# Optimization experiments

Hardware: AMD Instinct MI355X
Metric: run time of the kernel (lower is better)

Reference implementation:

```python
import jax, jax.numpy as jnp
import numpy as np

E = 1024      # hidden_size
H = 16        # num_heads
D = E // H    # head_dim = 64
WIN = 256     # window_size
STRIDE = 128
G = 1         # global_tokens
B = 2
L = 4097      # seq_len; local_seq_len = 4096 tiles exactly into 31 windows


def setup_inputs() -> dict:
    key = jax.random.key(0)
    ks = jax.random.split(key, 9)
    s = 0.02
    return {
        "hidden_states": jax.random.normal(ks[0], (B, L, E), jnp.float32),
        "Wq": jax.random.normal(ks[1], (E, E), jnp.float32) * s,
        "bq": jnp.zeros((E,), jnp.float32),
        "Wk": jax.random.normal(ks[2], (E, E), jnp.float32) * s,
        "bk": jnp.zeros((E,), jnp.float32),
        "Wv": jax.random.normal(ks[3], (E, E), jnp.float32) * s,
        "bv": jnp.zeros((E,), jnp.float32),
        "Wo": jax.random.normal(ks[4], (E, E), jnp.float32) * s,
        "bo": jnp.zeros((E,), jnp.float32),
    }


def reference(hidden_states, Wq, bq, Wk, bk, Wv, bv, Wo, bo):
    b, seq_len, e = hidden_states.shape
    scale = 1.0 / jnp.sqrt(jnp.asarray(D, hidden_states.dtype))

    q = (hidden_states @ Wq + bq).reshape(b, seq_len, H, D)
    k = (hidden_states @ Wk + bk).reshape(b, seq_len, H, D)
    v = (hidden_states @ Wv + bv).reshape(b, seq_len, H, D)

    # ---- global tokens attend to the full sequence ----
    qg = q[:, :G]                                        # [b, G, H, D]
    gw = jnp.einsum('bghd,bshd->bhgs', qg, k) * scale    # [b, H, G, L]
    gp = jax.nn.softmax(gw, axis=-1)
    gctx = jnp.einsum('bhgs,bshd->bghd', gp, v).reshape(b, G, e)

    # ---- local windowed attention (overlapping strided windows) ----
    ql, kl, vl = q[:, G:], k[:, G:], v[:, G:]
    Lc = seq_len - G                                     # 4096
    num_windows = max(1, (Lc - WIN) // STRIDE + 1)       # 31
    starts = jnp.arange(num_windows) * STRIDE
    widx = starts[:, None] + jnp.arange(WIN)             # [W, w] window indices

    qw = ql[:, widx]                                     # [b, W, w, H, D]
    kw = kl[:, widx]
    vw = vl[:, widx]
    aw = jnp.einsum('bwqhd,bwkhd->bwhqk', qw, kw) * scale  # [b, W, H, w, w]
    ap = jax.nn.softmax(aw, axis=-1)
    ctx = jnp.einsum('bwhqk,bwkhd->bwqhd', ap, vw)       # [b, W, w, H, D]
    ctx = ctx.reshape(b, num_windows * WIN, e)

    flat = widx.reshape(-1)                              # [W*w]
    local = jnp.zeros((b, Lc, e), hidden_states.dtype).at[:, flat].add(ctx)
    counts = jnp.zeros((Lc,), hidden_states.dtype).at[flat].add(1.0)
    counts = jnp.maximum(counts, 1.0)
    local = local / counts[None, :, None]                # average over overlaps

    out = jnp.concatenate([gctx, local], axis=1)         # [b, L, E]
    return out @ Wo + bo
```

## Files before the change

kernel.cpp:

```cpp
#include <hip/hip_runtime.h>

typedef unsigned short u16;
typedef unsigned int u32;
typedef __bf16 bf16x8 __attribute__((ext_vector_type(8)));
typedef float f4_t __attribute__((ext_vector_type(4)));

#define E_DIM 1024
#define L_TOT 4097
#define B_SZ 2
#define M_ROWS 8194
#define NWIN 31
#define HHEADS 16
#define GCHUNKS 17

__device__ __forceinline__ float b2f(u16 v) {
  union { u32 u; float f; } x; x.u = ((u32)v) << 16; return x.f;
}
__device__ __forceinline__ u16 f2b(float f) {
  union { float f; u32 u; } x; x.f = f;
  u32 r = (x.u + 0x7FFFu + ((x.u >> 16) & 1u)) >> 16;
  return (u16)r;
}
__device__ __forceinline__ f4_t mfma16(bf16x8 a, bf16x8 b, f4_t c) {
  return __builtin_amdgcn_mfma_f32_16x16x32_bf16(a, b, c, 0, 0, 0);
}
__device__ __forceinline__ u32 cvtpk(float lo, float hi) {
  u32 r;
  asm volatile("v_cvt_pk_bf16_f32 %0, %1, %2" : "=v"(r) : "v"(lo), "v"(hi));
  return r;
}

#define GLOAD16(gp, lp)                                                              \
  __builtin_amdgcn_global_load_lds(                                                  \
      (const __attribute__((address_space(1))) u32*)(gp),                            \
      (__attribute__((address_space(3))) u32*)(lp), 16, 0, 0)

#define WAITVM(N) asm volatile("s_waitcnt vmcnt(" #N ")" ::: "memory")

__global__ __launch_bounds__(256) void cvt_kernel(const float* __restrict__ src,
                                                  u16* __restrict__ dst, int n4) {
  int i = blockIdx.x * 256 + threadIdx.x;
  if (i >= n4) return;
  float4 v = ((const float4*)src)[i];
  u16 o[4] = {f2b(v.x), f2b(v.y), f2b(v.z), f2b(v.w)};
  *(uint2*)(dst + (size_t)i * 4) = *(uint2*)o;
}

__global__ __launch_bounds__(256) void wtrans_kernel(const float* __restrict__ w0,
                                                     const float* __restrict__ w1,
                                                     const float* __restrict__ w2,
                                                     const float* __restrict__ w3,
                                                     u16* __restrict__ wtb) {
  const float* src = blockIdx.z == 0 ? w0 : blockIdx.z == 1 ? w1 : blockIdx.z == 2 ? w2 : w3;
  u16* dst = wtb + (size_t)blockIdx.z * E_DIM * E_DIM;
  __shared__ float tile[32][33];
  int tx = threadIdx.x, ty = threadIdx.y;
  int x = blockIdx.x * 32 + tx;
  int y0 = blockIdx.y * 32;
  for (int j = ty; j < 32; j += 8) tile[j][tx] = src[(size_t)(y0 + j) * E_DIM + x];
  __syncthreads();
  for (int j = ty; j < 32; j += 8)
    dst[(size_t)(blockIdx.x * 32 + j) * E_DIM + blockIdx.y * 32 + tx] = f2b(tile[tx][j]);
}

template <int MODE, int BN>
__global__ __launch_bounds__(256) void gemmB_kernel(const u16* __restrict__ A,
                                                    const u16* __restrict__ Wt,
                                                    const float* __restrict__ b0,
                                                    const float* __restrict__ b1,
                                                    const float* __restrict__ b2,
                                                    void* __restrict__ outBase,
                                                    int M, int NTIL) {
  constexpr int NB = BN / 32;
  constexpr int ABUF = 128 * 64;
  constexpr int BBUF = BN * 64;
  __shared__ __align__(16) u16 sm[2 * ABUF + 2 * BBUF];
  u16* sA = sm;
  u16* sB = sm + 2 * ABUF;
  u16* epi16 = sm;
  float* epi32 = (float*)sm;

  int nwg = gridDim.x;
  int q8 = nwg >> 3, r8 = nwg & 7;
  int orig = blockIdx.x;
  int xcd = orig & 7, loc = orig >> 3;
  int wg = (xcd < r8 ? xcd * (q8 + 1) : r8 * (q8 + 1) + (xcd - r8) * q8) + loc;
  int mt = wg / NTIL, nt = wg - mt * NTIL;
  int m0 = mt * 128, n0 = nt * BN;

  int t = threadIdx.x, lane = t & 63, w = t >> 6;
  int wr = w >> 1, wc = w & 1;
  int lr = lane & 15, g = lane >> 4;

  int rsub = t >> 3;
  int ssrc = ((t & 7) ^ (rsub & 7)) * 8;
  int wbase = w * 512;
  const u16* pa[4];
  const u16* pb[NB];
#pragma unroll
  for (int c = 0; c < 4; c++) {
    int ra = m0 + c * 32 + rsub;
    if (ra >= M) ra = M - 1;
    pa[c] = A + (size_t)ra * 1024 + ssrc;
  }
#pragma unroll
  for (int c = 0; c < NB; c++) pb[c] = Wt + (size_t)(n0 + c * 32 + rsub) * 1024 + ssrc;

#define STAGE(bf, kt)                                                      \
  {                                                                        \
    int ko_ = (kt) * 64;                                                   \
    _Pragma("unroll") for (int c_ = 0; c_ < 4; c_++)                       \
        GLOAD16(pa[c_] + ko_, sA + (bf) * ABUF + c_ * 2048 + wbase);       \
    _Pragma("unroll") for (int c_ = 0; c_ < NB; c_++)                      \
        GLOAD16(pb[c_] + ko_, sB + (bf) * BBUF + c_ * 2048 + wbase);       \
  }

#define COMPUTE(bf)                                                            \
  {                                                                            \
    _Pragma("unroll") for (int kk_ = 0; kk_ < 2; kk_++) {                      \
      int sl_ = ((kk_ * 4 + g) ^ (lr & 7)) * 8;                                \
      bf16x8 av_[4], bv_[NB];                                                  \
      _Pragma("unroll") for (int i_ = 0; i_ < 4; i_++)                         \
          av_[i_] = *(const bf16x8*)&sA[(bf) * ABUF + (wr * 64 + i_ * 16 + lr) * 64 + sl_]; \
      _Pragma("unroll") for (int j_ = 0; j_ < NB; j_++)                        \
          bv_[j_] = *(const bf16x8*)&sB[(bf) * BBUF + (wc * (BN / 2) + j_ * 16 + lr) * 64 + sl_]; \
      _Pragma("unroll") for (int i_ = 0; i_ < 4; i_++)                         \
        _Pragma("unroll") for (int j_ = 0; j_ < NB; j_++)                      \
            acc[i_][j_] = mfma16(av_[i_], bv_[j_], acc[i_][j_]);               \
    }                                                                          \
  }

  f4_t acc[4][NB] = {};

  STAGE(0, 0);
  STAGE(1, 1);

  int buf = 0;
  for (int kt = 0; kt < 16; ++kt) {
    if (kt < 15) {
      if constexpr (NB == 4) { WAITVM(8); } else { WAITVM(6); }
    } else {
      WAITVM(0);
    }
    __builtin_amdgcn_sched_barrier(0);
    __builtin_amdgcn_s_barrier();
    __builtin_amdgcn_sched_barrier(0);
    COMPUTE(buf);
    __builtin_amdgcn_sched_barrier(0);
    __builtin_amdgcn_s_barrier();
    __builtin_amdgcn_sched_barrier(0);
    if (kt < 14) STAGE(buf, kt + 2);
    buf ^= 1;
  }
  __syncthreads();

  if (MODE == 0) {
    int tsel = n0 >> 10, ncb = n0 & 1023;
    const float* bp = tsel == 0 ? b0 : (tsel == 1 ? b1 : b2);
#pragma unroll
    for (int j = 0; j < NB; j++) {
      int ncl = wc * (BN / 2) + j * 16 + lr;
      float bb = bp[ncb + ncl];
#pragma unroll
      for (int i = 0; i < 4; i++) {
        int mlb = wr * 64 + i * 16 + g * 4;
#pragma unroll
        for (int r = 0; r < 4; r++) epi16[(mlb + r) * 136 + ncl] = f2b(acc[i][j][r] + bb);
      }
    }
    __syncthreads();
    int row = t >> 1, half = t & 1;
    int m = m0 + row;
    if (m < M) {
      u16* op = (u16*)outBase + (size_t)tsel * ((size_t)M_ROWS * E_DIM) + (size_t)m * E_DIM + ncb + half * 64;
      const u16* lp = epi16 + row * 136 + half * 64;
#pragma unroll
      for (int qd = 0; qd < 8; qd++) ((uint4*)op)[qd] = ((const uint4*)lp)[qd];
    }
  } else {
#pragma unroll
    for (int j = 0; j < NB; j++) {
      int ncl = wc * (BN / 2) + j * 16 + lr;
      float bb = b0[n0 + ncl];
#pragma unroll
      for (int i = 0; i < 4; i++) {
        int mlb = wr * 64 + i * 16 + g * 4;
#pragma unroll
        for (int r = 0; r < 4; r++) epi32[(mlb + r) * 68 + ncl] = acc[i][j][r] + bb;
      }
    }
    __syncthreads();
    int row = t >> 1, half = t & 1;
    int m = m0 + row;
    if (m < M) {
      float* op = (float*)outBase + (size_t)m * E_DIM + n0 + half * 32;
      const float* lp = epi32 + row * 68 + half * 32;
#pragma unroll
      for (int qd = 0; qd < 8; qd++) ((float4*)op)[qd] = ((const float4*)lp)[qd];
    }
  }
#undef STAGE
#undef COMPUTE
}

__global__ __launch_bounds__(256) void gattn1_kernel(const u16* __restrict__ Qb,
                                                     const u16* __restrict__ Kb,
                                                     const u16* __restrict__ Vb,
                                                     float* __restrict__ part) {
  int c = blockIdx.x;
  int h = blockIdx.y;
  int b = blockIdx.z;
  int t = threadIdx.x;
  __shared__ float qsh[64];
  __shared__ float red[4];
  __shared__ float psh[256];
  __shared__ float cred[4][64];

  size_t base = (size_t)b * L_TOT * E_DIM + h * 64;
  if (t < 64) qsh[t] = b2f(Qb[base + t]);
  __syncthreads();

  int row = c * 256 + t;
  bool valid = row < L_TOT;
  float dot = -1e30f;
  if (valid) {
    const u16* kp = Kb + base + (size_t)row * E_DIM;
    float acc = 0.f;
#pragma unroll
    for (int j = 0; j < 64; j += 8) {
      uint4 kv = *(const uint4*)(kp + j);
      const u16* kk = (const u16*)&kv;
#pragma unroll
      for (int q = 0; q < 8; q++) acc += qsh[j + q] * b2f(kk[q]);
    }
    dot = acc * 0.125f;
  }
  float m = dot;
  for (int mask = 1; mask < 64; mask <<= 1) m = fmaxf(m, __shfl_xor(m, mask));
  if ((t & 63) == 0) red[t >> 6] = m;
  __syncthreads();
  m = fmaxf(fmaxf(red[0], red[1]), fmaxf(red[2], red[3]));
  float p = valid ? __expf(dot - m) : 0.f;
  psh[t] = p;
  float s = p;
  for (int mask = 1; mask < 64; mask <<= 1) s += __shfl_xor(s, mask);
  __syncthreads();
  if ((t & 63) == 0) red[t >> 6] = s;
  __syncthreads();
  s = red[0] + red[1] + red[2] + red[3];

  int d = t & 63, gq = t >> 6;
  float acc = 0.f;
#pragma unroll 4
  for (int i = 0; i < 64; i++) {
    int sl = gq * 64 + i;
    int r2 = c * 256 + sl;
    if (r2 < L_TOT) acc += psh[sl] * b2f(Vb[base + (size_t)r2 * E_DIM + d]);
  }
  cred[gq][d] = acc;
  __syncthreads();
  if (t < 64) {
    float v = cred[0][t] + cred[1][t] + cred[2][t] + cred[3][t];
    float* pp = part + (((size_t)(b * HHEADS + h) * GCHUNKS + c) * 66);
    pp[t] = v;
    if (t == 0) { pp[64] = m; pp[65] = s; }
  }
}

__global__ __launch_bounds__(64) void gattn2_kernel(const float* __restrict__ part,
                                                    u16* __restrict__ ctxb) {
  int bh = blockIdx.x;
  int b = bh >> 4, h = bh & 15;
  int d = threadIdx.x;
  const float* pp = part + ((size_t)(b * HHEADS + h) * GCHUNKS) * 66;
  float m = -1e30f;
#pragma unroll
  for (int c = 0; c < GCHUNKS; c++) m = fmaxf(m, pp[c * 66 + 64]);
  float stot = 0.f, acc = 0.f;
#pragma unroll
  for (int c = 0; c < GCHUNKS; c++) {
    float w = __expf(pp[c * 66 + 64] - m);
    stot += pp[c * 66 + 65] * w;
    acc += pp[c * 66 + d] * w;
  }
  ctxb[(size_t)b * L_TOT * E_DIM + h * 64 + d] = f2b(acc / stot);
}

#define VT_IDX(d, k) ((d) * 264 + ((k) ^ ((((d) >> 3) & 7) << 3)))
__global__ __launch_bounds__(256) void wattn_kernel(const u16* __restrict__ Qb,
                                                    const u16* __restrict__ Kb,
                                                    const u16* __restrict__ Vb,
                                                    u16* __restrict__ winctx) {
  int wdw = blockIdx.x;
  int h = blockIdx.y;
  int b = blockIdx.z;

  __shared__ __align__(16) u16 Ks[256 * 64];
  __shared__ __align__(16) u16 Vt[64 * 264];

  int t = threadIdx.x, lane = t & 63, wv = t >> 6;
  int g = lane >> 4, lr = lane & 15;
  size_t rowbase = (size_t)b * L_TOT + 1 + (size_t)wdw * 128;
  int hoff = h * 64;

  {
    int rsub = t >> 3;
    int ssrc = ((t & 7) ^ (rsub & 7)) * 8;
    const u16* kp = Kb + (rowbase + rsub) * E_DIM + hoff + ssrc;
#pragma unroll
    for (int c = 0; c < 8; c++)
      GLOAD16(kp + (size_t)c * 32 * E_DIM, Ks + c * 2048 + wv * 512);
  }
#pragma unroll
  for (int rep = 0; rep < 8; rep++) {
    int u = rep * 256 + t;
    int i = u >> 3;
    int d0 = (u & 7) * 8;
    uint4 v = *(const uint4*)(Vb + (rowbase + i) * E_DIM + hoff + d0);
    const u16* pv = (const u16*)&v;
#pragma unroll
    for (int j = 0; j < 8; j++) Vt[VT_IDX(d0 + j, i)] = pv[j];
  }
  __syncthreads();

  int slo = (2 * (g & 1)) * 16 + lr;
  int shi = slo + 16;

  for (int grp = 0; grp < 4; grp++) {
    int q0 = grp * 64 + wv * 16;
    const u16* qp = Qb + (rowbase + q0 + lr) * E_DIM + hoff;
    bf16x8 qa0 = *(const bf16x8*)(qp + g * 8);
    bf16x8 qa1 = *(const bf16x8*)(qp + 32 + g * 8);

    f4_t s[16];
    __builtin_amdgcn_s_setprio(1);
#pragma unroll
    for (int ki = 0; ki < 16; ki++) {
      int row = ki * 16 + lr;
      bf16x8 ka0 = *(const bf16x8*)&Ks[row * 64 + ((g ^ (lr & 7)) << 3)];
      bf16x8 ka1 = *(const bf16x8*)&Ks[row * 64 + (((4 + g) ^ (lr & 7)) << 3)];
      f4_t z = {};
      z = mfma16(ka0, qa0, z);
      z = mfma16(ka1, qa1, z);
      s[ki] = z;
    }
    __builtin_amdgcn_s_setprio(0);

    float mx = -1e30f;
#pragma unroll
    for (int ki = 0; ki < 16; ki++) {
      mx = fmaxf(mx, fmaxf(fmaxf(s[ki][0], s[ki][1]), fmaxf(s[ki][2], s[ki][3])));
    }
    mx = fmaxf(mx, __shfl_xor(mx, 16));
    mx = fmaxf(mx, __shfl_xor(mx, 32));
    float mx8 = mx * 0.125f;
    float sum = 0.f;
    u32 pk[16][2];
#pragma unroll
    for (int ki = 0; ki < 16; ki++) {
      float p0 = __expf(fmaf(s[ki][0], 0.125f, -mx8));
      float p1 = __expf(fmaf(s[ki][1], 0.125f, -mx8));
      float p2 = __expf(fmaf(s[ki][2], 0.125f, -mx8));
      float p3 = __expf(fmaf(s[ki][3], 0.125f, -mx8));
      sum += (p0 + p1) + (p2 + p3);
      pk[ki][0] = cvtpk(p0, p1);
      pk[ki][1] = cvtpk(p2, p3);
    }
    sum += __shfl_xor(sum, 16);
    sum += __shfl_xor(sum, 32);
    float inv = 1.0f / sum;

    u32 paw[8][4];
    bool hi = g >= 2;
#pragma unroll
    for (int kt = 0; kt < 8; kt++) {
      u32 v00 = __shfl((int)pk[kt * 2][0], slo);
      u32 v01 = __shfl((int)pk[kt * 2][1], slo);
      u32 v10 = __shfl((int)pk[kt * 2 + 1][0], slo);
      u32 v11 = __shfl((int)pk[kt * 2 + 1][1], slo);
      u32 w00 = __shfl((int)pk[kt * 2][0], shi);
      u32 w01 = __shfl((int)pk[kt * 2][1], shi);
      u32 w10 = __shfl((int)pk[kt * 2 + 1][0], shi);
      u32 w11 = __shfl((int)pk[kt * 2 + 1][1], shi);
      paw[kt][0] = hi ? v10 : v00;
      paw[kt][1] = hi ? v11 : v01;
      paw[kt][2] = hi ? w10 : w00;
      paw[kt][3] = hi ? w11 : w01;
    }

    f4_t o[4] = {};
    __builtin_amdgcn_s_setprio(1);
#pragma unroll
    for (int dtile = 0; dtile < 4; dtile++) {
      int d = dtile * 16 + lr;
      int dswz = (((d >> 3) & 7) << 3);
#pragma unroll
      for (int kt = 0; kt < 8; kt++) {
        int kphys = (kt * 32 + g * 8) ^ dswz;
        bf16x8 vb = *(const bf16x8*)&Vt[d * 264 + kphys];
        o[dtile] = mfma16(*(const bf16x8*)&paw[kt][0], vb, o[dtile]);
      }
    }
    __builtin_amdgcn_s_setprio(0);

    float invr[4];
#pragma unroll
    for (int r = 0; r < 4; r++) invr[r] = __shfl(inv, g * 4 + r);
    size_t orow = (size_t)(b * NWIN + wdw) * 256 + q0;
#pragma unroll
    for (int dtile = 0; dtile < 4; dtile++) {
#pragma unroll
      for (int r = 0; r < 4; r++) {
        winctx[(orow + g * 4 + r) * E_DIM + hoff + dtile * 16 + lr] =
            f2b(o[dtile][r] * invr[r]);
      }
    }
  }
}

__global__ __launch_bounds__(256) void combine_kernel(const u16* __restrict__ winctx,
                                                      u16* __restrict__ ctxb) {
  int idx = blockIdx.x * 256 + threadIdx.x;
  int e0 = (idx & 127) * 8;
  int p = (idx >> 7) & 4095;
  int b = idx >> 19;
  int whi = p >> 7;
  if (whi > 30) whi = 30;
  int off_hi = p - whi * 128;
  int wlo = whi - 1;
  bool has_lo = (wlo >= 0) && (off_hi < 128);

  uint4 vhi = *(const uint4*)(winctx + (((size_t)(b * NWIN + whi) * 256 + off_hi) * E_DIM) + e0);
  const u16* ph = (const u16*)&vhi;
  float vals[8];
#pragma unroll
  for (int j = 0; j < 8; j++) vals[j] = b2f(ph[j]);
  if (has_lo) {
    uint4 vlo = *(const uint4*)(winctx + (((size_t)(b * NWIN + wlo) * 256 + off_hi + 128) * E_DIM) + e0);
    const u16* pl = (const u16*)&vlo;
#pragma unroll
    for (int j = 0; j < 8; j++) vals[j] = (vals[j] + b2f(pl[j])) * 0.5f;
  }
  u16 out[8];
#pragma unroll
  for (int j = 0; j < 8; j++) out[j] = f2b(vals[j]);
  *(uint4*)(ctxb + ((size_t)b * L_TOT + 1 + p) * E_DIM + e0) = *(uint4*)out;
}

extern "C" void kernel_launch(void* const* d_in, const int* in_sizes, int n_in,
                              void* d_out, int out_size, void* d_ws, size_t ws_size,
                              hipStream_t stream) {
  const float* hs = (const float*)d_in[0];
  const float* Wq = (const float*)d_in[1];
  const float* bq = (const float*)d_in[2];
  const float* Wk = (const float*)d_in[3];
  const float* bk = (const float*)d_in[4];
  const float* Wv = (const float*)d_in[5];
  const float* bv = (const float*)d_in[6];
  const float* Wo = (const float*)d_in[7];
  const float* bo = (const float*)d_in[8];

  const size_t BLE = (size_t)M_ROWS * E_DIM;
  const size_t BLE_B = BLE * 2;
  const size_t EE = (size_t)E_DIM * E_DIM;

  char* ws = (char*)d_ws;
  u16* hsb = (u16*)(ws);
  u16* wtb = (u16*)(ws + BLE_B);
  u16* qkv = (u16*)(ws + BLE_B + 4 * EE * 2);
  u16* Qb = qkv;
  u16* Kb = qkv + BLE;
  u16* Vb = qkv + 2 * BLE;
  u16* ctxb = (u16*)(ws + BLE_B + 4 * EE * 2 + 3 * BLE_B);
  u16* winctx = (u16*)(ws + BLE_B + 4 * EE * 2 + 4 * BLE_B);
  float* gpart = (float*)(ws + BLE_B + 4 * EE * 2 + 4 * BLE_B +
                          (size_t)B_SZ * NWIN * 256 * E_DIM * 2);

  cvt_kernel<<<8194, 256, 0, stream>>>(hs, hsb, (int)(BLE / 4));
  wtrans_kernel<<<dim3(32, 32, 4), dim3(32, 8), 0, stream>>>(Wq, Wk, Wv, Wo, wtb);
  gemmB_kernel<0, 128><<<65 * 24, 256, 0, stream>>>(hsb, wtb, bq, bk, bv, qkv, M_ROWS, 24);
  gattn1_kernel<<<dim3(GCHUNKS, HHEADS, B_SZ), 256, 0, stream>>>(Qb, Kb, Vb, gpart);
  gattn2_kernel<<<32, 64, 0, stream>>>(gpart, ctxb);
  wattn_kernel<<<dim3(NWIN, HHEADS, B_SZ), 256, 0, stream>>>(Qb, Kb, Vb, winctx);
  combine_kernel<<<4096, 256, 0, stream>>>(winctx, ctxb);
  gemmB_kernel<1, 64><<<65 * 16, 256, 0, stream>>>(ctxb, wtb + 3 * EE, bo, bo, bo, d_out, M_ROWS, 16);
}
```

Before: 224.4 us.

## Rework GEMM kernels with BK=32 double buffering, smaller LDS, and higher occupancy

Replaces the templated GEMM with a new body that stages 32-wide K slices instead of 64, cutting shared memory to about 34KB so four workgroups can share a CU (launch_bounds 256,4). LDS fragments are loaded before the barrier, the next stage is issued, and MFMAs run at raised priority, which overlaps copies with compute. The output projection now uses 128x128 tiles with a two-pass fp32 epilogue, and the XCD remap is simplified. The aim is better latency hiding and fewer redundant A-tile loads, at the cost of twice as many barriers per K.

Result: faster. 215.0 us (-4.2%).

```diff
diff --git a/kernel.cpp b/kernel.cpp
--- a/kernel.cpp
+++ b/kernel.cpp
@@ -63,144 +63,166 @@
     dst[(size_t)(blockIdx.x * 32 + j) * E_DIM + blockIdx.y * 32 + tx] = f2b(tile[tx][j]);
 }
 
-template <int MODE, int BN>
-__global__ __launch_bounds__(256) void gemmB_kernel(const u16* __restrict__ A,
+template <int MODE>
+__device__ __forceinline__ void gemmC_body(const u16* __restrict__ A,
+                                           const u16* __restrict__ Wt,
+                                           const float* __restrict__ b0,
+                                           const float* __restrict__ b1,
+                                           const float* __restrict__ b2,
+                                           void* __restrict__ outBase,
+                                           int M, int NTIL) {
+  __shared__ __align__(16) char smraw[34816];
+  u16* sA = (u16*)smraw;
+  u16* sB = sA + 2 * 4096;
+  u16* epi16 = (u16*)smraw;
+  float* epi32 = (float*)smraw;
+
+  int nwg = gridDim.x;
+  int cpx = nwg >> 3;
+  int orig = blockIdx.x;
+  int wg = (orig & 7) * cpx + (orig >> 3);
+  int mt = wg / NTIL, nt = wg - mt * NTIL;
+  int m0 = mt * 128, n0 = nt * 128;
+
+  int t = threadIdx.x, lane = t & 63, w = t >> 6;
+  int wr = w >> 1, wc = w & 1;
+  int lr = lane & 15, g = lane >> 4;
+
+  int ssrc = (((t & 3) ^ ((t >> 3) & 3)) << 3);
+  const u16* pa[2];
+  const u16* pb[2];
+#pragma unroll
+  for (int c = 0; c < 2; c++) {
+    int ra = m0 + c * 64 + (t >> 2);
+    if (ra >= M) ra = M - 1;
+    pa[c] = A + (size_t)ra * 1024 + ssrc;
+    pb[c] = Wt + (size_t)(n0 + c * 64 + (t >> 2)) * 1024 + ssrc;
+  }
+  int wb = w * 512;
+
+#define STAGE(bf, ks)                                              \
+  {                                                                \
+    GLOAD16(pa[0] + (ks) * 32, sA + (bf) * 4096 + wb);             \
+    GLOAD16(pa[1] + (ks) * 32, sA + (bf) * 4096 + 2048 + wb);      \
+    GLOAD16(pb[0] + (ks) * 32, sB + (bf) * 4096 + wb);             \
+    GLOAD16(pb[1] + (ks) * 32, sB + (bf) * 4096 + 2048 + wb);      \
+  }
+
+  int swz = ((g ^ ((lr >> 1) & 3)) << 3);
+  int arow0 = wr * 64 + lr;
+  int brow0 = wc * 64 + lr;
+
+  f4_t acc[4][4] = {};
+
+  STAGE(0, 0);
+  STAGE(1, 1);
+  WAITVM(4);
+  __builtin_amdgcn_s_barrier();
+  __builtin_amdgcn_sched_barrier(0);
+
+#pragma unroll 2
+  for (int ks = 0; ks < 32; ++ks) {
+    int bf = ks & 1;
+    int base = bf * 4096;
+    bf16x8 av[4], bv[4];
+#pragma unroll
+    for (int i = 0; i < 4; i++)
+      av[i] = *(const bf16x8*)&sA[base + (arow0 + i * 16) * 32 + swz];
+#pragma unroll
+    for (int j = 0; j < 4; j++)
+      bv[j] = *(const bf16x8*)&sB[base + (brow0 + j * 16) * 32 + swz];
+    __syncthreads();
+    if (ks < 30) STAGE(bf, ks + 2);
+    __builtin_amdgcn_sched_barrier(0);
+    __builtin_amdgcn_s_setprio(1);
+#pragma unroll
+    for (int i = 0; i < 4; i++)
+#pragma unroll
+      for (int j = 0; j < 4; j++) acc[i][j] = mfma16(av[i], bv[j], acc[i][j]);
+    __builtin_amdgcn_s_setprio(0);
+    if (ks < 30) {
+      WAITVM(4);
+    } else if (ks == 30) {
+      WAITVM(0);
+    }
+    if (ks < 31) {
+      __builtin_amdgcn_s_barrier();
+      __builtin_amdgcn_sched_barrier(0);
+    }
+  }
+  __syncthreads();
+
+  if (MODE == 0) {
+    int tsel = n0 >> 10, ncb = n0 & 1023;
+    const float* bp = tsel == 0 ? b0 : (tsel == 1 ? b1 : b2);
+#pragma unroll
+    for (int j = 0; j < 4; j++) {
+      int ncl = wc * 64 + j * 16 + lr;
+      float bb = bp[ncb + ncl];
+#pragma unroll
+      for (int i = 0; i < 4; i++) {
+        int mlb = wr * 64 + i * 16 + g * 4;
+#pragma unroll
+        for (int r = 0; r < 4; r++) epi16[(mlb + r) * 136 + ncl] = f2b(acc[i][j][r] + bb);
+      }
+    }
+    __syncthreads();
+    int row = t >> 1, half = t & 1;
+    int m = m0 + row;
+    if (m < M) {
+      u16* op = (u16*)outBase + (size_t)tsel * ((size_t)M_ROWS * E_DIM) + (size_t)m * E_DIM + ncb + half * 64;
+      const u16* lp = epi16 + row * 136 + half * 64;
+#pragma unroll
+      for (int qd = 0; qd < 8; qd++) ((uint4*)op)[qd] = ((const uint4*)lp)[qd];
+    }
+  } else {
+#pragma unroll
+    for (int p = 0; p < 2; p++) {
+      if (p) __syncthreads();
+      if (wc == p) {
+#pragma unroll
+        for (int j = 0; j < 4; j++) {
+          int ncl = j * 16 + lr;
+          float bb = b0[n0 + p * 64 + ncl];
+#pragma unroll
+          for (int i = 0; i < 4; i++) {
+            int mlb = wr * 64 + i * 16 + g * 4;
+#pragma unroll
+            for (int r = 0; r < 4; r++) epi32[(mlb + r) * 68 + ncl] = acc[i][j][r] + bb;
+          }
+        }
+      }
+      __syncthreads();
+      int row = t >> 1, qr = t & 1;
+      int m = m0 + row;
+      if (m < M) {
+        float* op = (float*)outBase + (size_t)m * E_DIM + n0 + p * 64 + qr * 32;
+        const float* lp = epi32 + row * 68 + qr * 32;
+#pragma unroll
+        for (int qd = 0; qd < 8; qd++) ((float4*)op)[qd] = ((const float4*)lp)[qd];
+      }
+    }
+  }
+#undef STAGE
+}
+
+__global__ __launch_bounds__(256, 4) void gemmC_qkv(const u16* __restrict__ A,
                                                     const u16* __restrict__ Wt,
                                                     const float* __restrict__ b0,
                                                     const float* __restrict__ b1,
                                                     const float* __restrict__ b2,
                                                     void* __restrict__ outBase,
                                                     int M, int NTIL) {
-  constexpr int NB = BN / 32;
-  constexpr int ABUF = 128 * 64;
-  constexpr int BBUF = BN * 64;
-  __shared__ __align__(16) u16 sm[2 * ABUF + 2 * BBUF];
-  u16* sA = sm;
-  u16* sB = sm + 2 * ABUF;
-  u16* epi16 = sm;
-  float* epi32 = (float*)sm;
-
-  int nwg = gridDim.x;
-  int q8 = nwg >> 3, r8 = nwg & 7;
-  int orig = blockIdx.x;
-  int xcd = orig & 7, loc = orig >> 3;
-  int wg = (xcd < r8 ? xcd * (q8 + 1) : r8 * (q8 + 1) + (xcd - r8) * q8) + loc;
-  int mt = wg / NTIL, nt = wg - mt * NTIL;
-  int m0 = mt * 128, n0 = nt * BN;
-
-  int t = threadIdx.x, lane = t & 63, w = t >> 6;
-  int wr = w >> 1, wc = w & 1;
-  int lr = lane & 15, g = lane >> 4;
-
-  int rsub = t >> 3;
-  int ssrc = ((t & 7) ^ (rsub & 7)) * 8;
-  int wbase = w * 512;
-  const u16* pa[4];
-  const u16* pb[NB];
-#pragma unroll
-  for (int c = 0; c < 4; c++) {
-    int ra = m0 + c * 32 + rsub;
-    if (ra >= M) ra = M - 1;
-    pa[c] = A + (size_t)ra * 1024 + ssrc;
-  }
-#pragma unroll
-  for (int c = 0; c < NB; c++) pb[c] = Wt + (size_t)(n0 + c * 32 + rsub) * 1024 + ssrc;
-
-#define STAGE(bf, kt)                                                      \
-  {                                                                        \
-    int ko_ = (kt) * 64;                                                   \
-    _Pragma("unroll") for (int c_ = 0; c_ < 4; c_++)                       \
-        GLOAD16(pa[c_] + ko_, sA + (bf) * ABUF + c_ * 2048 + wbase);       \
-    _Pragma("unroll") for (int c_ = 0; c_ < NB; c_++)                      \
-        GLOAD16(pb[c_] + ko_, sB + (bf) * BBUF + c_ * 2048 + wbase);       \
-  }
-
-#define COMPUTE(bf)                                                            \
-  {                                                                            \
-    _Pragma("unroll") for (int kk_ = 0; kk_ < 2; kk_++) {                      \
-      int sl_ = ((kk_ * 4 + g) ^ (lr & 7)) * 8;                                \
-      bf16x8 av_[4], bv_[NB];                                                  \
-      _Pragma("unroll") for (int i_ = 0; i_ < 4; i_++)                         \
-          av_[i_] = *(const bf16x8*)&sA[(bf) * ABUF + (wr * 64 + i_ * 16 + lr) * 64 + sl_]; \
-      _Pragma("unroll") for (int j_ = 0; j_ < NB; j_++)                        \
-          bv_[j_] = *(const bf16x8*)&sB[(bf) * BBUF + (wc * (BN / 2) + j_ * 16 + lr) * 64 + sl_]; \
-      _Pragma("unroll") for (int i_ = 0; i_ < 4; i_++)                         \
-        _Pragma("unroll") for (int j_ = 0; j_ < NB; j_++)                      \
-            acc[i_][j_] = mfma16(av_[i_], bv_[j_], acc[i_][j_]);               \
-    }                                                                          \
-  }
-
-  f4_t acc[4][NB] = {};
-
-  STAGE(0, 0);
-  STAGE(1, 1);
-
-  int buf = 0;
-  for (int kt = 0; kt < 16; ++kt) {
-    if (kt < 15) {
-      if constexpr (NB == 4) { WAITVM(8); } else { WAITVM(6); }
-    } else {
-      WAITVM(0);
-    }
-    __builtin_amdgcn_sched_barrier(0);
-    __builtin_amdgcn_s_barrier();
-    __builtin_amdgcn_sched_barrier(0);
-    COMPUTE(buf);
-    __builtin_amdgcn_sched_barrier(0);
-    __builtin_amdgcn_s_barrier();
-    __builtin_amdgcn_sched_barrier(0);
-    if (kt < 14) STAGE(buf, kt + 2);
-    buf ^= 1;
-  }
-  __syncthreads();
-
-  if (MODE == 0) {
-    int tsel = n0 >> 10, ncb = n0 & 1023;
-    const float* bp = tsel == 0 ? b0 : (tsel == 1 ? b1 : b2);
-#pragma unroll
-    for (int j = 0; j < NB; j++) {
-      int ncl = wc * (BN / 2) + j * 16 + lr;
-      float bb = bp[ncb + ncl];
-#pragma unroll
-      for (int i = 0; i < 4; i++) {
-        int mlb = wr * 64 + i * 16 + g * 4;
-#pragma unroll
-        for (int r = 0; r < 4; r++) epi16[(mlb + r) * 136 + ncl] = f2b(acc[i][j][r] + bb);
-      }
-    }
-    __syncthreads();
-    int row = t >> 1, half = t & 1;
-    int m = m0 + row;
-    if (m < M) {
-      u16* op = (u16*)outBase + (size_t)tsel * ((size_t)M_ROWS * E_DIM) + (size_t)m * E_DIM + ncb + half * 64;
-      const u16* lp = epi16 + row * 136 + half * 64;
-#pragma unroll
-      for (int qd = 0; qd < 8; qd++) ((uint4*)op)[qd] = ((const uint4*)lp)[qd];
-    }
-  } else {
-#pragma unroll
-    for (int j = 0; j < NB; j++) {
-      int ncl = wc * (BN / 2) + j * 16 + lr;
-      float bb = b0[n0 + ncl];
-#pragma unroll
-      for (int i = 0; i < 4; i++) {
-        int mlb = wr * 64 + i * 16 + g * 4;
-#pragma unroll
-        for (int r = 0; r < 4; r++) epi32[(mlb + r) * 68 + ncl] = acc[i][j][r] + bb;
-      }
-    }
-    __syncthreads();
-    int row = t >> 1, half = t & 1;
-    int m = m0 + row;
-    if (m < M) {
-      float* op = (float*)outBase + (size_t)m * E_DIM + n0 + half * 32;
-      const float* lp = epi32 + row * 68 + half * 32;
-#pragma unroll
-      for (int qd = 0; qd < 8; qd++) ((float4*)op)[qd] = ((const float4*)lp)[qd];
-    }
-  }
-#undef STAGE
-#undef COMPUTE
+  gemmC_body<0>(A, Wt, b0, b1, b2, outBase, M, NTIL);
+}
+__global__ __launch_bounds__(256, 4) void gemmC_out(const u16* __restrict__ A,
+                                                    const u16* __restrict__ Wt,
+                                                    const float* __restrict__ b0,
+                                                    const float* __restrict__ b1,
+                                                    const float* __restrict__ b2,
+                                                    void* __restrict__ outBase,
+                                                    int M, int NTIL) {
+  gemmC_body<1>(A, Wt, b0, b1, b2, outBase, M, NTIL);
 }
 
 __global__ __launch_bounds__(256) void gattn1_kernel(const u16* __restrict__ Qb,
@@ -478,10 +500,10 @@
 
   cvt_kernel<<<8194, 256, 0, stream>>>(hs, hsb, (int)(BLE / 4));
   wtrans_kernel<<<dim3(32, 32, 4), dim3(32, 8), 0, stream>>>(Wq, Wk, Wv, Wo, wtb);
-  gemmB_kernel<0, 128><<<65 * 24, 256, 0, stream>>>(hsb, wtb, bq, bk, bv, qkv, M_ROWS, 24);
+  gemmC_qkv<<<65 * 24, 256, 0, stream>>>(hsb, wtb, bq, bk, bv, qkv, M_ROWS, 24);
   gattn1_kernel<<<dim3(GCHUNKS, HHEADS, B_SZ), 256, 0, stream>>>(Qb, Kb, Vb, gpart);
   gattn2_kernel<<<32, 64, 0, stream>>>(gpart, ctxb);
   wattn_kernel<<<dim3(NWIN, HHEADS, B_SZ), 256, 0, stream>>>(Qb, Kb, Vb, winctx);
   combine_kernel<<<4096, 256, 0, stream>>>(winctx, ctxb);
-  gemmB_kernel<1, 64><<<65 * 16, 256, 0, stream>>>(ctxb, wtb + 3 * EE, bo, bo, bo, d_out, M_ROWS, 16);
-}
+  gemmC_out<<<65 * 8, 256, 0, stream>>>(ctxb, wtb + 3 * EE, bo, bo, bo, d_out, M_ROWS, 8);
+}
```
